# Optimization experiments

Measured on AMD Instinct MI355X. Metric: run time of the kernel, lower is better.

The kernel has to match this reference:

```python
import math
import jax, jax.numpy as jnp
import numpy as np

B, S, D = 2, 1024, 4096
H, DH = 32, 128


def setup_inputs() -> dict:
    key = jax.random.key(0)
    ks = jax.random.split(key, 8)
    scale = 1.0 / math.sqrt(D)
    return {
        "hidden_q": jax.random.normal(ks[0], (B, S, D), jnp.float32),
        "hidden_kv": jax.random.normal(ks[1], (B, S, D), jnp.float32),
        "attention_mask": jax.random.randint(ks[2], (B, S, S), 0, 2) > 0,
        "position_bias": jax.random.normal(ks[3], (B, H, S, S), jnp.float32),
        "Wq": jax.random.normal(ks[4], (D, H * DH), jnp.float32) * scale,
        "Wk": jax.random.normal(ks[5], (D, H * DH), jnp.float32) * scale,
        "Wv": jax.random.normal(ks[6], (D, H * DH), jnp.float32) * scale,
        "Wo": jax.random.normal(ks[7], (H * DH, D), jnp.float32) * scale,
    }


def reference(hidden_q, hidden_kv, attention_mask, position_bias, Wq, Wk, Wv, Wo):
    b, len_q, _ = hidden_q.shape
    len_k = hidden_kv.shape[1]
    # projections -> [B, H, S, DH]
    q = (hidden_q @ Wq).reshape(b, len_q, H, DH).transpose(0, 2, 1, 3)
    k = (hidden_kv @ Wk).reshape(b, len_k, H, DH).transpose(0, 2, 1, 3)
    v = (hidden_kv @ Wv).reshape(b, len_k, H, DH).transpose(0, 2, 1, 3)
    # scores [B, H, Q, K]
    score = jnp.einsum("bhqd,bhkd->bhqk", q, k) / math.sqrt(DH)
    score = score + position_bias
    mask = attention_mask[:, None, :, :]  # [B,1,Q,K]
    score = jnp.where(mask, score, -jnp.inf)
    probs = jax.nn.softmax(score, axis=-1)
    probs = jnp.where(mask, probs, 0.0)  # post-softmax mask (also kills NaN rows)
    ctx = jnp.einsum("bhqk,bhkd->bhqd", probs, v)
    ctx = ctx.transpose(0, 2, 1, 3).reshape(b, len_q, H * DH)
    out = ctx @ Wo
    return out
```

## Files before the change

kernel.cpp:

```cpp
#include <hip/hip_runtime.h>
#include <stdint.h>


#define B_  2
#define S_  1024
#define D_  4096
#define H_  32
#define DH_ 128
#define M_  (B_ * S_)
#define KSTR 8192

typedef __attribute__((ext_vector_type(8))) short bf16x8;
typedef __attribute__((ext_vector_type(4))) float f32x4;

static __device__ __forceinline__ unsigned short f32_to_bf16(float f) {
    unsigned int x = __float_as_uint(f);
    x += 0x7fffu + ((x >> 16) & 1u);
    return (unsigned short)(x >> 16);
}

static __device__ __forceinline__ f32x4 mfma16(bf16x8 a, bf16x8 b, f32x4 c) {
    return __builtin_amdgcn_mfma_f32_16x16x32_bf16(a, b, c, 0, 0, 0);
}

#if defined(__has_builtin)
#if __has_builtin(__builtin_amdgcn_global_load_lds)
#define HAVE_GLOAD_LDS 1
#endif
#endif

#ifdef HAVE_GLOAD_LDS
#define GLD16(g, lbase, lane)                                                  \
    __builtin_amdgcn_global_load_lds(                                          \
        (const __attribute__((address_space(1))) void*)(g),                    \
        (__attribute__((address_space(3))) void*)(lbase), 16, 0, 0)
#else
#define GLD16(g, lbase, lane)                                                  \
    do { *(bf16x8*)((unsigned short*)(lbase) + (size_t)(lane) * 8) =           \
             *(const bf16x8*)(g); } while (0)
#endif

__global__ void detect_mask_kernel(const unsigned char* __restrict__ m, int* flag) {
    int l = threadIdx.x;
    uint4 v = ((const uint4*)m)[l];
    unsigned int ww[4] = {v.x, v.y, v.z, v.w};
    int nz_hi = 0, nz_lo01 = 0;
#pragma unroll
    for (int wi = 0; wi < 4; ++wi)
#pragma unroll
        for (int bi = 0; bi < 4; ++bi) {
            unsigned int byte = (ww[wi] >> (bi * 8)) & 0xffu;
            if (byte && bi != 0) nz_hi = 1;
            if (byte && bi <= 1) nz_lo01 = 1;
        }
    int any_hi = __any(nz_hi);
    int any_lo01 = __any(nz_lo01);
    if (l == 0) *flag = (!any_hi) ? 1 : ((!any_lo01) ? 2 : 0);
}

__global__ void canon_mask_kernel(const void* __restrict__ m, const int* __restrict__ flag,
                                  unsigned char* __restrict__ out, int n) {
    int i = blockIdx.x * 256 + threadIdx.x;
    if (i >= n) return;
    int f = *flag;
    unsigned char v;
    if (f == 1)      v = (unsigned char)(((const int*)m)[i] != 0);
    else if (f == 2) v = (unsigned char)(((const float*)m)[i] != 0.0f);
    else             v = (unsigned char)(((const unsigned char*)m)[i] != 0);
    out[i] = v;
}

__global__ void cvt2_bf16_kernel(const float* __restrict__ a, const float* __restrict__ b,
                                 unsigned short* __restrict__ oa, unsigned short* __restrict__ ob) {
    int i = blockIdx.x * 256 + threadIdx.x;
    const int n4 = (B_ * S_ * D_) / 4;
    const float* src = (i < n4) ? a : b;
    unsigned short* dst = (i < n4) ? oa : ob;
    int j = (i < n4) ? i : i - n4;
    float4 v = ((const float4*)src)[j];
    ushort4 o;
    o.x = f32_to_bf16(v.x); o.y = f32_to_bf16(v.y);
    o.z = f32_to_bf16(v.z); o.w = f32_to_bf16(v.w);
    ((ushort4*)dst)[j] = o;
}

__global__ __launch_bounds__(256) void transpose_all_kernel(
        const float* __restrict__ Wq, const float* __restrict__ Wk,
        const float* __restrict__ Wv, const float* __restrict__ Wo,
        unsigned short* __restrict__ WTq, unsigned short* __restrict__ WTkv,
        unsigned short* __restrict__ WTo) {
    __shared__ unsigned short lds[64][65];
    int which = blockIdx.x >> 12;
    int bid = blockIdx.x & 4095;
    const float* W = (which == 0) ? Wq : (which == 1) ? Wk : (which == 2) ? Wv : Wo;
    unsigned short* WT = (which == 0) ? WTq
                       : (which == 1) ? WTkv
                       : (which == 2) ? (WTkv + (size_t)4096 * 4096)
                                      : WTo;
    int bx = bid & 63;
    int by = bid >> 6;
    int t = threadIdx.x;
    int tr = t >> 4;
    int tc = (t & 15) * 4;
#pragma unroll
    for (int p = 0; p < 4; ++p) {
        int r = p * 16 + tr;
        float4 v = *(const float4*)(W + (size_t)(by * 64 + r) * D_ + bx * 64 + tc);
        lds[r][tc + 0] = f32_to_bf16(v.x);
        lds[r][tc + 1] = f32_to_bf16(v.y);
        lds[r][tc + 2] = f32_to_bf16(v.z);
        lds[r][tc + 3] = f32_to_bf16(v.w);
    }
    __syncthreads();
#pragma unroll
    for (int p = 0; p < 4; ++p) {
        int n = p * 16 + tr;
        ushort4 o;
        o.x = lds[tc + 0][n]; o.y = lds[tc + 1][n];
        o.z = lds[tc + 2][n]; o.w = lds[tc + 3][n];
        *(ushort4*)(WT + (size_t)(bx * 64 + n) * D_ + by * 64 + tc) = o;
    }
}

__global__ __launch_bounds__(256) void vt_kernel(const unsigned short* __restrict__ KV,
                                                 unsigned short* __restrict__ Vtw) {
    __shared__ unsigned short lds[64][72];
    int bid = blockIdx.x;
    int dt = bid & 1;
    int st = (bid >> 1) & 15;
    int h  = (bid >> 5) & 31;
    int b  = bid >> 10;
    int t = threadIdx.x;
    int r = t >> 2;
    int c0 = (t & 3) * 16;
    const unsigned short* src =
        KV + (size_t)(b * S_ + st * 64 + r) * KSTR + 4096 + h * DH_ + dt * 64 + c0;
    bf16x8 v0 = *(const bf16x8*)(src);
    bf16x8 v1 = *(const bf16x8*)(src + 8);
    *(bf16x8*)&lds[r][c0] = v0;
    *(bf16x8*)&lds[r][c0 + 8] = v1;
    __syncthreads();
    unsigned short tmp[16];
#pragma unroll
    for (int i = 0; i < 16; ++i) tmp[i] = lds[c0 + i][r];
    unsigned short* dst =
        Vtw + ((size_t)((b * H_ + h) * DH_ + dt * 64 + r)) * S_ + st * 64 + c0;
    *(bf16x8*)dst = *(bf16x8*)&tmp[0];
    *(bf16x8*)(dst + 8) = *(bf16x8*)&tmp[8];
}

__device__ __forceinline__ void gemm_core(const unsigned short* __restrict__ A,
                                          const unsigned short* __restrict__ BT,
                                          void* __restrict__ C, int out_f32,
                                          int m0, int n0, int cstride,
                                          int koff, int NT, char* ldsc) {
    const int t = threadIdx.x;
    const int w = t >> 6, l = t & 63;
    const int lr = l & 15, lg = l >> 4;
    const int wmh = w >> 2;
    const int walf = w & 3;
    const int wm = wmh << 7;
    const int wn = walf << 6;

    const int ca0 = lg ^ (lr & 7);
    const int aoff0 = lr * 128 + (ca0 << 4);
    const int aoff1 = lr * 128 + ((ca0 ^ 4) << 4);
    const int boff0 = ((walf & 1) * 64 + lr) * 128 + (ca0 << 4);
    const int boff1 = ((walf & 1) * 64 + lr) * 128 + ((ca0 ^ 4) << 4);

    const int srow = t >> 3;
    const int sch = (t & 7) ^ (srow & 7);
    const size_t soff0 = (size_t)srow * 4096 + (size_t)(sch << 3);
    const size_t soff1 = soff0 + (size_t)64 * 4096;
    const int ldso = w << 10;

    f32x4 ac[8][4];
    f32x4 vzero = {0.f, 0.f, 0.f, 0.f};
#pragma unroll
    for (int i = 0; i < 8; ++i)
#pragma unroll
        for (int j = 0; j < 4; ++j) ac[i][j] = vzero;

#define STAGE_ELEM(E, SS)                                                      \
    do {                                                                       \
        int er_ = (E) & 3;                                                     \
        const unsigned short* mb_ = (er_ < 2)                                  \
            ? A + (size_t)(m0 + ((er_ & 1) << 7)) * 4096                       \
            : BT + (size_t)(n0 + ((er_ & 1) << 7)) * 4096;                     \
        mb_ += (size_t)((((E) >> 2) << 6) + koff);                             \
        char* d0_ = ldsc + (SS) * 16384 + ldso;                                \
        GLD16(mb_ + soff0, d0_, l);                                            \
        GLD16(mb_ + soff1, d0_ + 8192, l);                                     \
    } while (0)

#pragma unroll
    for (int e = 0; e < 5; ++e) STAGE_ELEM(e, e);

    const int NT4 = NT << 2;
    int E = 5, ss = 5, s0 = 0;
    bf16x8 bfr[4][2];

#pragma unroll 1
    for (int tau = 0; tau < NT; ++tau) {
        int sA = s0 + wmh;          if (sA >= 9) sA -= 9;
        int sB = s0 + 2 + (walf >> 1); if (sB >= 9) sB -= 9;
        const char* pA0 = ldsc + sA * 16384 + aoff0;
        const char* pA1 = ldsc + sA * 16384 + aoff1;
        const char* pB0 = ldsc + sB * 16384 + boff0;
        const char* pB1 = ldsc + sB * 16384 + boff1;
#pragma unroll
        for (int r = 0; r < 4; ++r) {
            if (r == 0) {
                if (tau == NT - 1)
                    asm volatile("s_waitcnt vmcnt(0)" ::: "memory");
                else
                    asm volatile("s_waitcnt vmcnt(2)" ::: "memory");
            }
            __builtin_amdgcn_s_barrier();
            asm volatile("" ::: "memory");
            if (r == 0) {
#pragma unroll
                for (int nf = 0; nf < 4; ++nf) {
                    bfr[nf][0] = *(const bf16x8*)(pB0 + nf * 2048);
                    bfr[nf][1] = *(const bf16x8*)(pB1 + nf * 2048);
                }
            }
            bf16x8 af[2][2];
            int mfb = r << 1;
#pragma unroll
            for (int j = 0; j < 2; ++j) {
                af[j][0] = *(const bf16x8*)(pA0 + (mfb + j) * 2048);
                af[j][1] = *(const bf16x8*)(pA1 + (mfb + j) * 2048);
            }
            if (E < NT4) STAGE_ELEM(E, ss);
            ++E; ss = (ss == 8) ? 0 : ss + 1;
            __builtin_amdgcn_s_setprio(1);
#pragma unroll
            for (int j = 0; j < 2; ++j)
#pragma unroll
                for (int nf = 0; nf < 4; ++nf) {
                    ac[mfb + j][nf] = mfma16(af[j][0], bfr[nf][0], ac[mfb + j][nf]);
                    ac[mfb + j][nf] = mfma16(af[j][1], bfr[nf][1], ac[mfb + j][nf]);
                }
            __builtin_amdgcn_s_setprio(0);
        }
        s0 += 4; if (s0 >= 9) s0 -= 9;
    }
#undef STAGE_ELEM

#pragma unroll
    for (int mf = 0; mf < 8; ++mf)
#pragma unroll
        for (int nf = 0; nf < 4; ++nf)
#pragma unroll
            for (int q = 0; q < 4; ++q) {
                int row = m0 + wm + mf * 16 + lg * 4 + q;
                int col = n0 + wn + nf * 16 + lr;
                if (out_f32)
                    ((float*)C)[(size_t)row * cstride + col] = ac[mf][nf][q];
                else
                    ((unsigned short*)C)[(size_t)row * cstride + col] = f32_to_bf16(ac[mf][nf][q]);
            }
}

__global__ __launch_bounds__(512, 2) void gemm_qkv_kernel(
        const unsigned short* __restrict__ Aq, const unsigned short* __restrict__ Bq,
        float* __restrict__ Pq,
        const unsigned short* __restrict__ Akv, const unsigned short* __restrict__ Bkv,
        unsigned short* __restrict__ Ckv) {
    __shared__ char ldsbuf[9 * 16384];
    int bid = blockIdx.x;
    if (bid < 256) {
        int bm = bid & 7, bn = bid >> 3;
        gemm_core(Akv, Bkv, Ckv, 0, bm << 8, bn << 8, 8192, 0, 64, ldsbuf);
    } else {
        int e = bid - 256;
        int bm = e & 7;
        int rest = e >> 3;
        int bn = rest & 15;
        int ks = rest >> 4;
        gemm_core(Aq, Bq, Pq + (size_t)ks * M_ * D_, 1, bm << 8, bn << 8, 4096,
                  ks * 2048, 32, ldsbuf);
    }
}

__global__ void reduce_q_kernel(const float* __restrict__ P, unsigned short* __restrict__ out) {
    int i = blockIdx.x * 256 + threadIdx.x;
    float4 a = ((const float4*)P)[i];
    float4 b = ((const float4*)(P + (size_t)M_ * D_))[i];
    ushort4 o;
    o.x = f32_to_bf16(a.x + b.x); o.y = f32_to_bf16(a.y + b.y);
    o.z = f32_to_bf16(a.z + b.z); o.w = f32_to_bf16(a.w + b.w);
    ((ushort4*)out)[i] = o;
}

__global__ __launch_bounds__(512, 2) void gemm_o_kernel(
        const unsigned short* __restrict__ A, const unsigned short* __restrict__ BT,
        float* __restrict__ P) {
    __shared__ char ldsbuf[9 * 16384];
    int bid = blockIdx.x;
    int bm = bid & 7;
    int rest = bid >> 3;
    int bn = rest & 15;
    int ks = rest >> 4;
    gemm_core(A, BT, P + (size_t)ks * M_ * D_, 1, bm << 8, bn << 8, 4096,
              ks * 2048, 32, ldsbuf);
}

__global__ void reduce_o_kernel(const float* __restrict__ P, float* __restrict__ out) {
    int i = blockIdx.x * 256 + threadIdx.x;
    float4 a = ((const float4*)P)[i];
    float4 b = ((const float4*)(P + (size_t)M_ * D_))[i];
    float4 o; o.x = a.x + b.x; o.y = a.y + b.y; o.z = a.z + b.z; o.w = a.w + b.w;
    ((float4*)out)[i] = o;
}

#define NEGF (-1e30f)
__global__ __launch_bounds__(256, 2) void attn_kernel(const unsigned short* __restrict__ Qw,
                                                      const unsigned short* __restrict__ KV,
                                                      const unsigned short* __restrict__ Vtw,
                                                      const float* __restrict__ bias,
                                                      const unsigned char* __restrict__ maskc,
                                                      unsigned short* __restrict__ ctx) {
    __shared__ unsigned short Kbuf[2][64 * 128];
    __shared__ unsigned short Vbuf[2][128 * 64];
    __shared__ unsigned short Plds[4][16 * 72];

    int bid = blockIdx.x;
    int qt = bid & 15, h = (bid >> 4) & 31, b = bid >> 9;
    int t = threadIdx.x, w = t >> 6, l = t & 63;
    int lr = l & 15, lg = l >> 4;
    int q0 = (qt << 6) + (w << 4);

    bf16x8 qf[4];
    const unsigned short* Qp = Qw + ((size_t)(b * S_ + q0 + lr)) * D_ + h * DH_ + lg * 8;
#pragma unroll
    for (int kf = 0; kf < 4; ++kf) qf[kf] = *(const bf16x8*)(Qp + kf * 32);

    f32x4 o[8];
    f32x4 vzero = {0.f, 0.f, 0.f, 0.f};
#pragma unroll
    for (int i = 0; i < 8; ++i) o[i] = vzero;
    float m_run = NEGF, l_run = 0.f;

    const float* biasp = bias + (((size_t)(b * H_ + h)) << 20)
                              + (((size_t)(q0 + lr)) << 10);
    const unsigned char* mp = maskc + ((size_t)b << 20)
                              + (((size_t)(q0 + lr)) << 10);
    const unsigned short* Kg = KV + (size_t)(b * S_) * KSTR + h * DH_;
    const unsigned short* Vg = Vtw + (((size_t)(b * H_ + h)) * DH_) * S_;

    float4 br0[4], br1[4];
    unsigned int mr0[4], mr1[4];

#define STAGE_KV(KT, BUF)                                                          \
    do { int kv0_ = (KT) << 6;                                                     \
        _Pragma("unroll")                                                          \
        for (int c = 0; c < 4; ++c) {                                              \
            int seg = (w << 2) + c;                                                \
            int krow = (seg << 2) + (l >> 4);                                      \
            int kch = (l & 15) ^ (krow & 7);                                       \
            GLD16(Kg + (size_t)(kv0_ + krow) * KSTR + (kch << 3),                  \
                  &Kbuf[BUF][seg << 9], l);                                        \
            int vrow = (seg << 3) + (l >> 3);                                      \
            int vch = (l & 7) ^ (vrow & 7);                                        \
            GLD16(Vg + (size_t)vrow * S_ + kv0_ + (vch << 3),                      \
                  &Vbuf[BUF][seg << 9], l);                                        \
        }                                                                          \
    } while (0)

#define LOAD_BM(BR, MR, KT)                                                        \
    do { int kv0_ = (KT) << 6;                                                     \
        _Pragma("unroll")                                                          \
        for (int nb = 0; nb < 4; ++nb) {                                           \
            BR[nb] = *(const float4*)(biasp + kv0_ + (nb << 4) + (lg << 2));       \
            MR[nb] = *(const unsigned int*)(mp + kv0_ + (nb << 4) + (lg << 2));    \
        }                                                                          \
    } while (0)

#define COMPUTE(BUF, BR, MR)                                                       \
    do {                                                                           \
        f32x4 s_[4];                                                               \
        __builtin_amdgcn_s_setprio(1);                                             \
        _Pragma("unroll")                                                          \
        for (int nb = 0; nb < 4; ++nb) {                                           \
            s_[nb] = vzero;                                                        \
            int krow = (nb << 4) + lr;                                             \
            _Pragma("unroll")                                                      \
            for (int kf = 0; kf < 4; ++kf) {                                       \
                int ba = ((krow << 8) + (((kf << 5) + (lg << 3)) << 1))            \
                         ^ ((krow & 7) << 4);                                      \
                bf16x8 kfr = *(const bf16x8*)((const char*)Kbuf[BUF] + ba);        \
                s_[nb] = mfma16(kfr, qf[kf], s_[nb]);    \
            }                                                                      \
        }                                                                          \
        __builtin_amdgcn_s_setprio(0);                                             \
        float sv[4][4];                                                            \
        _Pragma("unroll")                                                          \
        for (int nb = 0; nb < 4; ++nb) {                                           \
            float bb[4] = {BR[nb].x, BR[nb].y, BR[nb].z, BR[nb].w};                \
            _Pragma("unroll")                                                      \
            for (int r = 0; r < 4; ++r) {                                          \
                float x = fmaf(s_[nb][r], 0.08838834764831845f, bb[r]);            \
                sv[nb][r] = ((MR[nb] >> (r * 8)) & 0xffu) ? x : NEGF;              \
            }                                                                      \
        }                                                                          \
                         \
        float mt = sv[0][0];                                                       \
        _Pragma("unroll")                                                          \
        for (int nb = 0; nb < 4; ++nb)                                             \
            _Pragma("unroll")                                                      \
            for (int r = 0; r < 4; ++r) mt = fmaxf(mt, sv[nb][r]);                 \
        mt = fmaxf(mt, __shfl_xor(mt, 16, 64));                                    \
        mt = fmaxf(mt, __shfl_xor(mt, 32, 64));                                    \
        float mn = fmaxf(m_run, mt);                                               \
        float al = __expf(m_run - mn);                                             \
        m_run = mn;                                                                \
        float rs = 0.f;                                                            \
        _Pragma("unroll")                                                          \
        for (int nb = 0; nb < 4; ++nb)                                             \
            _Pragma("unroll")                                                      \
            for (int r = 0; r < 4; ++r) {                                          \
                sv[nb][r] = __expf(sv[nb][r] - m_run);                             \
                rs += sv[nb][r];                                                   \
            }                                                                      \
        rs += __shfl_xor(rs, 16, 64);                                              \
        rs += __shfl_xor(rs, 32, 64);                                              \
        l_run = l_run * al + rs;                                                   \
         \
        float alm[4];                                                              \
        _Pragma("unroll")                                                          \
        for (int r = 0; r < 4; ++r) alm[r] = __shfl(al, (lg << 2) + r, 64);        \
        _Pragma("unroll")                                                          \
        for (int nb2 = 0; nb2 < 8; ++nb2) {                                        \
            o[nb2][0] *= alm[0]; o[nb2][1] *= alm[1];                              \
            o[nb2][2] *= alm[2]; o[nb2][3] *= alm[3];                              \
        }                                                                          \
                                     \
        _Pragma("unroll")                                                          \
        for (int nb = 0; nb < 4; ++nb)                                             \
            _Pragma("unroll")                                                      \
            for (int r = 0; r < 4; ++r)                                            \
                Plds[w][lr * 72 + (nb << 4) + (lg << 2) + r] = f32_to_bf16(sv[nb][r]); \
        __builtin_amdgcn_s_setprio(1);                                             \
        _Pragma("unroll")                                                          \
        for (int kf2 = 0; kf2 < 2; ++kf2) {                                        \
            bf16x8 pf = *(const bf16x8*)&Plds[w][lr * 72 + (kf2 << 5) + (lg << 3)]; \
            _Pragma("unroll")                                                      \
            for (int nb2 = 0; nb2 < 8; ++nb2) {                                    \
                int dh = (nb2 << 4) + lr;                                          \
                int ba = ((dh << 7) + (((kf2 << 5) + (lg << 3)) << 1))             \
                         ^ ((dh & 7) << 4);                                        \
                bf16x8 vf = *(const bf16x8*)((const char*)Vbuf[BUF] + ba);         \
                o[nb2] = mfma16(pf, vf, o[nb2]);                                   \
            }                                                                      \
        }                                                                          \
        __builtin_amdgcn_s_setprio(0);                                             \
    } while (0)

    STAGE_KV(0, 0);
    LOAD_BM(br0, mr0, 0);

#pragma unroll 1
    for (int kt = 0; kt < 16; kt += 2) {
        __syncthreads();
        STAGE_KV(kt + 1, 1);
        LOAD_BM(br1, mr1, kt + 1);
        COMPUTE(0, br0, mr0);
        __syncthreads();
        if (kt < 14) {
            STAGE_KV(kt + 2, 0);
            LOAD_BM(br0, mr0, kt + 2);
        }
        COMPUTE(1, br1, mr1);
    }

    float lm[4];
#pragma unroll
    for (int r = 0; r < 4; ++r) lm[r] = __shfl(l_run, (lg << 2) + r, 64);
#pragma unroll
    for (int r = 0; r < 4; ++r) {
        float inv = lm[r] > 0.f ? 1.0f / lm[r] : 0.f;
        int q = q0 + (lg << 2) + r;
        unsigned short* cp = ctx + ((size_t)(b * S_ + q)) * D_ + h * DH_ + lr;
#pragma unroll
        for (int nb2 = 0; nb2 < 8; ++nb2)
            cp[nb2 * 16] = f32_to_bf16(o[nb2][r] * inv);
    }
#undef STAGE_KV
#undef LOAD_BM
#undef COMPUTE
}

extern "C" void kernel_launch(void* const* d_in, const int* in_sizes, int n_in,
                              void* d_out, int out_size, void* d_ws, size_t ws_size,
                              hipStream_t stream) {
    const float* hq   = (const float*)d_in[0];
    const float* hkv  = (const float*)d_in[1];
    const void*  mask = d_in[2];
    const float* bias = (const float*)d_in[3];
    const float* Wq   = (const float*)d_in[4];
    const float* Wk   = (const float*)d_in[5];
    const float* Wv   = (const float*)d_in[6];
    const float* Wo   = (const float*)d_in[7];
    float* out = (float*)d_out;

    char* ws = (char*)d_ws;
    unsigned char* mask_c = (unsigned char*)ws;
    int* flag             = (int*)(ws + (2u << 20));
    unsigned short* hq_b  = (unsigned short*)(ws + (2u << 20) + 4096);
    unsigned short* hkv_b = hq_b + ((size_t)1 << 23);
    unsigned short* WTq   = hkv_b + ((size_t)1 << 23);
    unsigned short* WTo   = WTq + ((size_t)1 << 24);
    unsigned short* WTkv  = WTo + ((size_t)1 << 24);
    unsigned short* Qws   = WTkv + ((size_t)1 << 25);
    unsigned short* KVws  = Qws + ((size_t)1 << 23);
    unsigned short* Cws   = KVws + ((size_t)1 << 24);
    unsigned short* Vtw   = Cws + ((size_t)1 << 23);
    float* Pws            = (float*)(Vtw + ((size_t)1 << 23));

    detect_mask_kernel<<<1, 64, 0, stream>>>((const unsigned char*)mask, flag);
    canon_mask_kernel<<<8192, 256, 0, stream>>>(mask, flag, mask_c, B_ * S_ * S_);
    cvt2_bf16_kernel<<<16384, 256, 0, stream>>>(hq, hkv, hq_b, hkv_b);
    transpose_all_kernel<<<16384, 256, 0, stream>>>(Wq, Wk, Wv, Wo, WTq, WTkv, WTo);

    gemm_qkv_kernel<<<512, 512, 0, stream>>>(hq_b, WTq, Pws, hkv_b, WTkv, KVws);
    reduce_q_kernel<<<(M_ * D_) / 1024, 256, 0, stream>>>(Pws, Qws);

    vt_kernel<<<B_ * H_ * 16 * 2, 256, 0, stream>>>(KVws, Vtw);
    attn_kernel<<<B_ * H_ * (S_ / 64), 256, 0, stream>>>(Qws, KVws, Vtw, bias, mask_c, Cws);

    gemm_o_kernel<<<256, 512, 0, stream>>>(Cws, WTo, Pws);
    reduce_o_kernel<<<(M_ * D_) / 1024, 256, 0, stream>>>(Pws, out);
}
```

Before: 504.8 us.

## Single-buffer attention K/V staging to raise occupancy to three blocks per CU

Replaces the double-buffered K/V LDS tiles and the two bias/mask register sets with single buffers, and raises launch bounds from 2 to 3 blocks per CU. The loop now computes on the current tile, synchronizes, then issues loads for the next tile. The aim is to hide latency through more resident waves instead of explicit software pipelining. The cost is that loads no longer overlap compute within a block, and register pressure is capped harder.

```diff
diff --git a/kernel.cpp b/kernel.cpp
--- a/kernel.cpp
+++ b/kernel.cpp
@@ -316,14 +316,14 @@
 }
 
 #define NEGF (-1e30f)
-__global__ __launch_bounds__(256, 2) void attn_kernel(const unsigned short* __restrict__ Qw,
+__global__ __launch_bounds__(256, 3) void attn_kernel(const unsigned short* __restrict__ Qw,
                                                       const unsigned short* __restrict__ KV,
                                                       const unsigned short* __restrict__ Vtw,
                                                       const float* __restrict__ bias,
                                                       const unsigned char* __restrict__ maskc,
                                                       unsigned short* __restrict__ ctx) {
-    __shared__ unsigned short Kbuf[2][64 * 128];
-    __shared__ unsigned short Vbuf[2][128 * 64];
+    __shared__ unsigned short Kbuf[64 * 128];
+    __shared__ unsigned short Vbuf[128 * 64];
     __shared__ unsigned short Plds[4][16 * 72];
 
     int bid = blockIdx.x;
@@ -350,10 +350,10 @@
     const unsigned short* Kg = KV + (size_t)(b * S_) * KSTR + h * DH_;
     const unsigned short* Vg = Vtw + (((size_t)(b * H_ + h)) * DH_) * S_;
 
-    float4 br0[4], br1[4];
-    unsigned int mr0[4], mr1[4];
-
-#define STAGE_KV(KT, BUF)                                                          \
+    float4 br[4];
+    unsigned int mr[4];
+
+#define STAGE_KV(KT)                                                               \
     do { int kv0_ = (KT) << 6;                                                     \
         _Pragma("unroll")                                                          \
         for (int c = 0; c < 4; ++c) {                                              \
@@ -361,24 +361,24 @@
             int krow = (seg << 2) + (l >> 4);                                      \
             int kch = (l & 15) ^ (krow & 7);                                       \
             GLD16(Kg + (size_t)(kv0_ + krow) * KSTR + (kch << 3),                  \
-                  &Kbuf[BUF][seg << 9], l);                                        \
+                  &Kbuf[seg << 9], l);                                             \
             int vrow = (seg << 3) + (l >> 3);                                      \
             int vch = (l & 7) ^ (vrow & 7);                                        \
             GLD16(Vg + (size_t)vrow * S_ + kv0_ + (vch << 3),                      \
-                  &Vbuf[BUF][seg << 9], l);                                        \
+                  &Vbuf[seg << 9], l);                                             \
         }                                                                          \
     } while (0)
 
-#define LOAD_BM(BR, MR, KT)                                                        \
+#define LOAD_BM(KT)                                                                \
     do { int kv0_ = (KT) << 6;                                                     \
         _Pragma("unroll")                                                          \
         for (int nb = 0; nb < 4; ++nb) {                                           \
-            BR[nb] = *(const float4*)(biasp + kv0_ + (nb << 4) + (lg << 2));       \
-            MR[nb] = *(const unsigned int*)(mp + kv0_ + (nb << 4) + (lg << 2));    \
+            br[nb] = *(const float4*)(biasp + kv0_ + (nb << 4) + (lg << 2));       \
+            mr[nb] = *(const unsigned int*)(mp + kv0_ + (nb << 4) + (lg << 2));    \
         }                                                                          \
     } while (0)
 
-#define COMPUTE(BUF, BR, MR)                                                       \
+#define COMPUTE()                                                                  \
     do {                                                                           \
         f32x4 s_[4];                                                               \
         __builtin_amdgcn_s_setprio(1);                                             \
@@ -390,22 +390,21 @@
             for (int kf = 0; kf < 4; ++kf) {                                       \
                 int ba = ((krow << 8) + (((kf << 5) + (lg << 3)) << 1))            \
                          ^ ((krow & 7) << 4);                                      \
-                bf16x8 kfr = *(const bf16x8*)((const char*)Kbuf[BUF] + ba);        \
-                s_[nb] = mfma16(kfr, qf[kf], s_[nb]);    \
+                bf16x8 kfr = *(const bf16x8*)((const char*)Kbuf + ba);             \
+                s_[nb] = mfma16(kfr, qf[kf], s_[nb]);                              \
             }                                                                      \
         }                                                                          \
         __builtin_amdgcn_s_setprio(0);                                             \
         float sv[4][4];                                                            \
         _Pragma("unroll")                                                          \
         for (int nb = 0; nb < 4; ++nb) {                                           \
-            float bb[4] = {BR[nb].x, BR[nb].y, BR[nb].z, BR[nb].w};                \
+            float bb[4] = {br[nb].x, br[nb].y, br[nb].z, br[nb].w};                \
             _Pragma("unroll")                                                      \
             for (int r = 0; r < 4; ++r) {                                          \
                 float x = fmaf(s_[nb][r], 0.08838834764831845f, bb[r]);            \
-                sv[nb][r] = ((MR[nb] >> (r * 8)) & 0xffu) ? x : NEGF;              \
+                sv[nb][r] = ((mr[nb] >> (r * 8)) & 0xffu) ? x : NEGF;              \
             }                                                                      \
         }                                                                          \
-                         \
         float mt = sv[0][0];                                                       \
         _Pragma("unroll")                                                          \
         for (int nb = 0; nb < 4; ++nb)                                             \
@@ -427,7 +426,6 @@
         rs += __shfl_xor(rs, 16, 64);                                              \
         rs += __shfl_xor(rs, 32, 64);                                              \
         l_run = l_run * al + rs;                                                   \
-         \
         float alm[4];                                                              \
         _Pragma("unroll")                                                          \
         for (int r = 0; r < 4; ++r) alm[r] = __shfl(al, (lg << 2) + r, 64);        \
@@ -436,7 +434,6 @@
             o[nb2][0] *= alm[0]; o[nb2][1] *= alm[1];                              \
             o[nb2][2] *= alm[2]; o[nb2][3] *= alm[3];                              \
         }                                                                          \
-                                     \
         _Pragma("unroll")                                                          \
         for (int nb = 0; nb < 4; ++nb)                                             \
             _Pragma("unroll")                                                      \
@@ -451,28 +448,25 @@
                 int dh = (nb2 << 4) + lr;                                          \
                 int ba = ((dh << 7) + (((kf2 << 5) + (lg << 3)) << 1))             \
                          ^ ((dh & 7) << 4);                                        \
-                bf16x8 vf = *(const bf16x8*)((const char*)Vbuf[BUF] + ba);         \
+                bf16x8 vf = *(const bf16x8*)((const char*)Vbuf + ba);              \
                 o[nb2] = mfma16(pf, vf, o[nb2]);                                   \
             }                                                                      \
         }                                                                          \
         __builtin_amdgcn_s_setprio(0);                                             \
     } while (0)
 
-    STAGE_KV(0, 0);
-    LOAD_BM(br0, mr0, 0);
+    STAGE_KV(0);
+    LOAD_BM(0);
 
 #pragma unroll 1
-    for (int kt = 0; kt < 16; kt += 2) {
+    for (int kt = 0; kt < 16; ++kt) {
         __syncthreads();
-        STAGE_KV(kt + 1, 1);
-        LOAD_BM(br1, mr1, kt + 1);
-        COMPUTE(0, br0, mr0);
+        COMPUTE();
         __syncthreads();
-        if (kt < 14) {
-            STAGE_KV(kt + 2, 0);
-            LOAD_BM(br0, mr0, kt + 2);
+        if (kt < 15) {
+            STAGE_KV(kt + 1);
+            LOAD_BM(kt + 1);
         }
-        COMPUTE(1, br1, mr1);
     }
 
     float lm[4];
```

Result: slower. 519.3 us (+2.9%).
